# Kernel optimization log

Measured on AMD Instinct MI355X. Metric: run time of the kernel, lower is better.

Reference implementation:

```python
import jax, jax.numpy as jnp
import numpy as np

TAU = 0.05


def _normalize(x):
    return x / jnp.linalg.norm(x, axis=-1, keepdims=True)


def setup_inputs() -> dict:
    key = jax.random.key(0)
    ks = jax.random.split(key, 7)
    D, S, Q, N, P = 256, 64, 4096, 16384, 1024
    return {
        "article_emb": jax.random.normal(ks[0], (D,), dtype=jnp.float32),
        "section_embs": jax.random.normal(ks[1], (S, D), dtype=jnp.float32),
        "question_embs": jax.random.normal(ks[2], (Q, D), dtype=jnp.float32),
        "sentence_embs": jax.random.normal(ks[3], (N, D), dtype=jnp.float32),
        "paragraph_idx_for_question": jax.random.randint(ks[4], (Q,), 0, P, dtype=jnp.int32),
        "section_idx_for_question": jax.random.randint(ks[5], (Q,), 0, S, dtype=jnp.int32),
        "sent_paragraph_idx": jax.random.randint(ks[6], (N,), 0, P, dtype=jnp.int32),
        "num_paragraphs": P,
    }


def reference(article_emb, section_embs, question_embs, sentence_embs,
              paragraph_idx_for_question, section_idx_for_question,
              sent_paragraph_idx, num_paragraphs):
    tau = TAU
    dt = question_embs.dtype
    # normalize (article is normalized in the original but unused in the loss; AT_loss == 0)
    _ = _normalize(article_emb)
    sec = _normalize(section_embs)   # [S, D]
    que = _normalize(question_embs)  # [Q, D]
    sen = _normalize(sentence_embs)  # [N, D]
    Q, N = que.shape[0], sen.shape[0]
    S = sec.shape[0]

    # ---------- QS debiased InfoNCE ----------
    sim_qs = jnp.matmul(que, sen.T) / tau              # [Q, N]
    exp_qs = jnp.exp(sim_qs)                           # [Q, N]
    pos = paragraph_idx_for_question[:, None] == sent_paragraph_idx[None, :]  # [Q, N]
    M = pos.sum(axis=1)                                # positives per question
    Nn = N - M                                         # negatives per question
    sum_pos = jnp.where(pos, exp_qs, 0.0).sum(axis=1)
    sum_neg = exp_qs.sum(axis=1) - sum_pos
    eta_plus = 1.0 / max(int(num_paragraphs), 1)
    eta_minus = 1.0 - eta_plus
    min_val = jnp.exp(jnp.asarray(-1.0 / tau, dtype=dt))
    M_f = jnp.maximum(M, 1).astype(dt)
    Nn_f = jnp.maximum(Nn, 1).astype(dt)
    g = jnp.maximum((sum_neg / Nn_f - eta_plus * sum_pos / M_f) / eta_minus, min_val)  # [Q]
    valid = (M > 0) & (Nn > 0)                         # [Q]
    # -log(numer / (numer + N_neg * g)) = -(sim - log(denom))
    denom_qs = exp_qs + (Nn.astype(dt) * g)[:, None]
    log_ratio_qs = sim_qs - jnp.log(denom_qs)
    mask_qs = pos & valid[:, None]
    total_qs = jnp.where(valid, M, 0).sum()
    qs_loss = -jnp.where(mask_qs, log_ratio_qs, 0.0).sum()
    qs_loss = jnp.where(total_qs > 0, qs_loss / total_qs.astype(dt), jnp.asarray(0.0, dt))

    # ---------- SQ InfoNCE ----------
    sim_sq = jnp.matmul(sec, que.T) / tau              # [S, Q]
    exp_sq = jnp.exp(sim_sq)
    posq = section_idx_for_question[None, :] == jnp.arange(S)[:, None]  # [S, Q]
    Mq = posq.sum(axis=1)
    Nnq = Q - Mq
    sum_neg_q = exp_sq.sum(axis=1) - jnp.where(posq, exp_sq, 0.0).sum(axis=1)  # [S]
    log_ratio_sq = sim_sq - jnp.log(exp_sq + sum_neg_q[:, None])
    validq = (Mq > 0) & (Nnq > 0)
    mask_sq = posq & validq[:, None]
    total_sq = jnp.where(validq, Mq, 0).sum()
    sq_loss = -jnp.where(mask_sq, log_ratio_sq, 0.0).sum()
    sq_loss = jnp.where(total_sq > 0, sq_loss / total_sq.astype(dt), jnp.asarray(0.0, dt))

    return qs_loss + sq_loss
```

## Files before the change

kernel.cpp:

```cpp
#include <hip/hip_runtime.h>
#include <hip/hip_bf16.h>
#include <math.h>

#define D 256
#define INV_TAU 20.0f
#define CAP 64
#define PBUF 128

typedef __attribute__((ext_vector_type(4))) float f32x4;
typedef __attribute__((ext_vector_type(8))) short bf16x8_t;

#define GLOAD16(gp, lp) \
    __builtin_amdgcn_global_load_lds((const __attribute__((address_space(1))) void*)(gp), \
                                     (__attribute__((address_space(3))) void*)(lp), 16, 0, 0)

__device__ __forceinline__ unsigned short f2bf(float f) {
    union { float f; unsigned u; } v; v.f = f;
    unsigned r = v.u + 0x7FFFu + ((v.u >> 16) & 1u);
    return (unsigned short)(r >> 16);
}

__global__ void norm_all(const float* __restrict__ que, const float* __restrict__ sen,
                         const float* __restrict__ sec,
                         unsigned short* __restrict__ queb, unsigned short* __restrict__ senb,
                         unsigned short* __restrict__ secb, int Q, int N, int S) {
    int r = blockIdx.x * 4 + (threadIdx.x >> 6);
    int lane = threadIdx.x & 63;
    if (r >= Q + N + S) return;
    const float* src; unsigned short* dst; int row;
    if (r < Q) { src = que; dst = queb; row = r; }
    else if (r < Q + N) { src = sen; dst = senb; row = r - Q; }
    else { src = sec; dst = secb; row = r - Q - N; }
    const float4* p = (const float4*)(src + (size_t)row * D);
    float4 v = p[lane];
    float ss = v.x * v.x + v.y * v.y + v.z * v.z + v.w * v.w;
    #pragma unroll
    for (int m = 1; m < 64; m <<= 1) ss += __shfl_xor(ss, m);
    float rn = rsqrtf(ss);
    ushort4 o;
    o.x = f2bf(v.x * rn); o.y = f2bf(v.y * rn); o.z = f2bf(v.z * rn); o.w = f2bf(v.w * rn);
    *(ushort4*)(dst + (size_t)row * D + lane * 4) = o;
}

__global__ __launch_bounds__(256, 4)
void qs_sq(const unsigned short* __restrict__ queb, const unsigned short* __restrict__ senb,
           const unsigned short* __restrict__ secb,
           const int* __restrict__ pidq, const int* __restrict__ pidn,
           const int* __restrict__ sidx, int Q,
           float* __restrict__ partial, int* __restrict__ cnt, float* __restrict__ pos_s,
           float* __restrict__ sq_all, float* __restrict__ sq_pos, int* __restrict__ sq_m,
           float* __restrict__ simq) {
    __shared__ unsigned short As[2][128 * 32];
    __shared__ unsigned short Bs[2][128 * 32];
    __shared__ int pqs[128];
    __shared__ int pns[128];
    __shared__ float sums[2][128];
    __shared__ int lcnt;
    __shared__ int lq[PBUF];
    __shared__ float lsv[PBUF];

    const int tid = threadIdx.x;
    const int lane = tid & 63;
    const int cl = lane & 15;
    const int g = lane >> 4;
    const int wid = tid >> 6;
    const int bid = blockIdx.x;
    const int nsq = Q >> 7;

    if (bid < nsq) {
        const int q0 = bid * 128;
        const int qw = q0 + wid * 32;
        f32x4 acc[4][2];
        #pragma unroll
        for (int si = 0; si < 4; ++si)
            #pragma unroll
            for (int qi = 0; qi < 2; ++qi)
                acc[si][qi] = (f32x4){0.f, 0.f, 0.f, 0.f};
        const unsigned short* abase = secb + (size_t)cl * D + g * 8;
        const unsigned short* bbase = queb + (size_t)(qw + cl) * D + g * 8;
        #pragma unroll
        for (int kk = 0; kk < 8; ++kk) {
            const int k0 = kk * 32;
            bf16x8_t af[4], bq[2];
            #pragma unroll
            for (int si = 0; si < 4; ++si)
                af[si] = *(const bf16x8_t*)(abase + si * 16 * D + k0);
            #pragma unroll
            for (int qi = 0; qi < 2; ++qi)
                bq[qi] = *(const bf16x8_t*)(bbase + qi * 16 * D + k0);
            #pragma unroll
            for (int si = 0; si < 4; ++si)
                #pragma unroll
                for (int qi = 0; qi < 2; ++qi)
                    acc[si][qi] = __builtin_amdgcn_mfma_f32_16x16x32_bf16(af[si], bq[qi], acc[si][qi], 0, 0, 0);
        }
        int sidxv[2];
        sidxv[0] = sidx[qw + cl];
        sidxv[1] = sidx[qw + 16 + cl];
        #pragma unroll
        for (int si = 0; si < 4; ++si) {
            float pa[4] = {0.f, 0.f, 0.f, 0.f};
            #pragma unroll
            for (int qi = 0; qi < 2; ++qi) {
                #pragma unroll
                for (int j = 0; j < 4; ++j) {
                    int srow = si * 16 + g * 4 + j;
                    float sv = acc[si][qi][j] * INV_TAU;
                    float e = __expf(sv);
                    pa[j] += e;
                    if (sidxv[qi] == srow) {
                        int q = qw + qi * 16 + cl;
                        simq[q] = sv;
                        atomicAdd(&sq_pos[srow], e);
                        atomicAdd(&sq_m[srow], 1);
                    }
                }
            }
            #pragma unroll
            for (int j = 0; j < 4; ++j) {
                float a = pa[j];
                #pragma unroll
                for (int msk = 1; msk < 16; msk <<= 1) a += __shfl_xor(a, msk);
                if (cl == 0) atomicAdd(&sq_all[si * 16 + g * 4 + j], a);
            }
        }
        return;
    }

    const int qbid = bid - nsq;
    const int xcd = qbid & 7;
    const int loc = qbid >> 3;
    const int qt = loc & 31;
    const int nt = xcd * 16 + (loc >> 5);
    const int wr = wid >> 1, wc = wid & 1;
    const int n0 = nt * 128;
    const int q0 = qt * 128;

    if (tid < 128) pqs[tid] = pidq[q0 + tid];
    else           pns[tid - 128] = pidn[n0 + tid - 128];
    if (tid == 0) lcnt = 0;
    __syncthreads();

    int cid0 = (2 * wid) * 64 + lane;
    int cid1 = (2 * wid + 1) * 64 + lane;
    int r0 = cid0 >> 2, c0 = cid0 & 3;
    int r1 = cid1 >> 2, c1 = cid1 & 3;
    const unsigned short* qa0 = queb + (size_t)(q0 + r0) * D + ((c0 ^ ((r0 >> 1) & 3)) << 3);
    const unsigned short* qa1 = queb + (size_t)(q0 + r1) * D + ((c1 ^ ((r1 >> 1) & 3)) << 3);
    const unsigned short* sb0 = senb + (size_t)(n0 + r0) * D + ((c0 ^ ((r0 >> 1) & 3)) << 3);
    const unsigned short* sb1 = senb + (size_t)(n0 + r1) * D + ((c1 ^ ((r1 >> 1) & 3)) << 3);
    const int ld0 = (2 * wid) * 512;
    const int ld1 = (2 * wid + 1) * 512;

#define STAGE(buf, k0) do { \
    GLOAD16(qa0 + (k0), &As[buf][ld0]); \
    GLOAD16(qa1 + (k0), &As[buf][ld1]); \
    GLOAD16(sb0 + (k0), &Bs[buf][ld0]); \
    GLOAD16(sb1 + (k0), &Bs[buf][ld1]); \
} while (0)

    f32x4 acc[4][4];
    #pragma unroll
    for (int m = 0; m < 4; ++m)
        #pragma unroll
        for (int n = 0; n < 4; ++n)
            acc[m][n] = (f32x4){0.f, 0.f, 0.f, 0.f};

    int offA[4], offB[4];
    #pragma unroll
    for (int m = 0; m < 4; ++m) {
        int r = wr * 64 + m * 16 + cl;
        offA[m] = r * 32 + ((g ^ ((r >> 1) & 3)) << 3);
    }
    #pragma unroll
    for (int n = 0; n < 4; ++n) {
        int r = wc * 64 + n * 16 + cl;
        offB[n] = r * 32 + ((g ^ ((r >> 1) & 3)) << 3);
    }

    STAGE(0, 0);
    #pragma unroll
    for (int ks = 0; ks < 8; ++ks) {
        const int cur = ks & 1;
        if (ks < 7) {
            STAGE(cur ^ 1, (ks + 1) * 32);
            asm volatile("s_waitcnt vmcnt(4)" ::: "memory");
        } else {
            asm volatile("s_waitcnt vmcnt(0)" ::: "memory");
        }
        __builtin_amdgcn_s_barrier();
        bf16x8_t af[4], bg[4];
        #pragma unroll
        for (int m = 0; m < 4; ++m) af[m] = *(const bf16x8_t*)&As[cur][offA[m]];
        #pragma unroll
        for (int n = 0; n < 4; ++n) bg[n] = *(const bf16x8_t*)&Bs[cur][offB[n]];
        #pragma unroll
        for (int m = 0; m < 4; ++m)
            #pragma unroll
            for (int n = 0; n < 4; ++n)
                acc[m][n] = __builtin_amdgcn_mfma_f32_16x16x32_bf16(af[m], bg[n], acc[m][n], 0, 0, 0);
        if (ks < 7) __builtin_amdgcn_s_barrier();
    }
#undef STAGE

    #pragma unroll
    for (int m = 0; m < 4; ++m) {
        float se[4] = {0.f, 0.f, 0.f, 0.f};
        int pqr[4];
        #pragma unroll
        for (int j = 0; j < 4; ++j) pqr[j] = pqs[wr * 64 + m * 16 + g * 4 + j];
        #pragma unroll
        for (int n = 0; n < 4; ++n) {
            const int pcol = pns[wc * 64 + n * 16 + cl];
            #pragma unroll
            for (int j = 0; j < 4; ++j) {
                float s = acc[m][n][j] * INV_TAU;
                float e = __expf(s);
                se[j] += e;
                if (pqr[j] == pcol) {
                    int li = atomicAdd(&lcnt, 1);
                    if (li < PBUF) { lq[li] = q0 + wr * 64 + m * 16 + g * 4 + j; lsv[li] = s; }
                }
            }
        }
        #pragma unroll
        for (int j = 0; j < 4; ++j) {
            float a = se[j];
            #pragma unroll
            for (int msk = 1; msk < 16; msk <<= 1) a += __shfl_xor(a, msk);
            if (cl == 0) sums[wc][wr * 64 + m * 16 + g * 4 + j] = a;
        }
    }
    __syncthreads();
    if (tid < 128)
        partial[(size_t)nt * Q + q0 + tid] = sums[0][tid] + sums[1][tid];
    int nc = lcnt < PBUF ? lcnt : PBUF;
    for (int i = tid; i < nc; i += 256) {
        int q = lq[i];
        int idx = atomicAdd(&cnt[q], 1);
        if (idx < CAP) pos_s[(size_t)q * CAP + idx] = lsv[i];
    }
}

__global__ __launch_bounds__(256)
void finish(const float* __restrict__ partial, int NB,
            const int* __restrict__ cnt, const float* __restrict__ pos_s,
            const int* __restrict__ sidx, const float* __restrict__ simq,
            const float* __restrict__ sq_all, const float* __restrict__ sq_pos,
            const int* __restrict__ sq_m,
            const int* __restrict__ npp, int Qn, int Ntot,
            float* __restrict__ bpart) {
    __shared__ float fred[4][4];
    const int tid = threadIdx.x, lane = tid & 63, wid = tid >> 6;
    const int q = blockIdx.x * 4 + wid;

    float Sa = 0.f;
    for (int nb = lane; nb < NB; nb += 64) Sa += partial[(size_t)nb * Qn + q];
    #pragma unroll
    for (int m = 1; m < 64; m <<= 1) Sa += __shfl_xor(Sa, m);

    int M = cnt[q];
    int mc = M < CAP ? M : CAP;
    float s = 0.f, e = 0.f;
    if (lane < mc) { s = pos_s[(size_t)q * CAP + lane]; e = __expf(s); }
    float Sp = e;
    #pragma unroll
    for (int m = 1; m < 64; m <<= 1) Sp += __shfl_xor(Sp, m);

    int Nn = Ntot - M;
    int P = npp[0];
    float eta_p = 1.0f / (float)(P > 1 ? P : 1);
    float eta_m = 1.0f - eta_p;
    float Mf = (float)(M > 1 ? M : 1);
    float Nnf = (float)(Nn > 1 ? Nn : 1);
    float gg = fmaxf(((Sa - Sp) / Nnf - eta_p * Sp / Mf) / eta_m, __expf(-INV_TAU));
    float c = (float)Nn * gg;

    float contrib = (lane < mc) ? (s - __logf(e + c)) : 0.f;
    #pragma unroll
    for (int m = 1; m < 64; m <<= 1) contrib += __shfl_xor(contrib, m);

    if (lane == 0) {
        float qs_num = 0.f, qs_cnt = 0.f, sq_num = 0.f, sq_cnt = 0.f;
        if (M > 0 && Nn > 0) { qs_num = contrib; qs_cnt = (float)M; }
        int sct = sidx[q];
        int Mq = sq_m[sct];
        if (Mq > 0 && (Qn - Mq) > 0) {
            float sv = simq[q];
            float sumneg = sq_all[sct] - sq_pos[sct];
            sq_num = sv - __logf(__expf(sv) + sumneg);
            sq_cnt = 1.f;
        }
        fred[wid][0] = qs_num; fred[wid][1] = qs_cnt;
        fred[wid][2] = sq_num; fred[wid][3] = sq_cnt;
    }
    __syncthreads();
    if (tid < 4) {
        float v = fred[0][tid] + fred[1][tid] + fred[2][tid] + fred[3][tid];
        bpart[(size_t)blockIdx.x * 4 + tid] = v;
    }
}

__global__ void combine2(const float* __restrict__ bpart, int nblk, float* __restrict__ out) {
    __shared__ float r2[4][4];
    const int tid = threadIdx.x, lane = tid & 63, wid = tid >> 6;
    float v[4] = {0.f, 0.f, 0.f, 0.f};
    for (int i = tid; i < nblk; i += 256) {
        #pragma unroll
        for (int c2 = 0; c2 < 4; ++c2) v[c2] += bpart[(size_t)i * 4 + c2];
    }
    #pragma unroll
    for (int m = 1; m < 64; m <<= 1)
        #pragma unroll
        for (int c2 = 0; c2 < 4; ++c2) v[c2] += __shfl_xor(v[c2], m);
    if (lane == 0) {
        #pragma unroll
        for (int c2 = 0; c2 < 4; ++c2) r2[wid][c2] = v[c2];
    }
    __syncthreads();
    if (tid == 0) {
        float qs_num = r2[0][0] + r2[1][0] + r2[2][0] + r2[3][0];
        float qs_cnt = r2[0][1] + r2[1][1] + r2[2][1] + r2[3][1];
        float sq_num = r2[0][2] + r2[1][2] + r2[2][2] + r2[3][2];
        float sq_cnt = r2[0][3] + r2[1][3] + r2[2][3] + r2[3][3];
        float qs = qs_cnt > 0.f ? -qs_num / qs_cnt : 0.f;
        float sq = sq_cnt > 0.f ? -sq_num / sq_cnt : 0.f;
        out[0] = qs + sq;
    }
}

extern "C" void kernel_launch(void* const* d_in, const int* in_sizes, int n_in,
                              void* d_out, int out_size, void* d_ws, size_t ws_size,
                              hipStream_t stream) {
    const float* sec = (const float*)d_in[1];
    const float* que = (const float*)d_in[2];
    const float* sen = (const float*)d_in[3];
    const int* pidq = (const int*)d_in[4];
    const int* sidx = (const int*)d_in[5];
    const int* pidn = (const int*)d_in[6];
    const int* npp = (const int*)d_in[7];
    const int S = in_sizes[1] / D;
    const int Q = in_sizes[2] / D;
    const int N = in_sizes[3] / D;
    const int NB = N / 128;
    const int FBLK = Q / 4;

    char* p = (char*)d_ws;
    unsigned short* queb = (unsigned short*)p; p += (size_t)Q * D * 2;
    unsigned short* senb = (unsigned short*)p; p += (size_t)N * D * 2;
    unsigned short* secb = (unsigned short*)p; p += (size_t)S * D * 2;
    float* simq = (float*)p; p += (size_t)Q * 4;
    float* pos_s = (float*)p; p += (size_t)Q * CAP * 4;
    float* partial = (float*)p; p += (size_t)NB * Q * 4;
    float* bpart = (float*)p; p += (size_t)FBLK * 4 * 4;
    char* z0 = p;
    int* cnt = (int*)p; p += (size_t)Q * 4;
    float* sq_all = (float*)p; p += (size_t)S * 4;
    float* sq_pos = (float*)p; p += (size_t)S * 4;
    int* sq_m = (int*)p; p += (size_t)S * 4;
    size_t zbytes = (size_t)(p - z0);

    hipMemsetAsync(z0, 0, zbytes, stream);
    norm_all<<<(Q + N + S + 3) / 4, 256, 0, stream>>>(que, sen, sec, queb, senb, secb, Q, N, S);
    qs_sq<<<Q / 128 + (Q / 128) * NB, 256, 0, stream>>>(queb, senb, secb, pidq, pidn, sidx, Q,
                                                        partial, cnt, pos_s,
                                                        sq_all, sq_pos, sq_m, simq);
    finish<<<FBLK, 256, 0, stream>>>(partial, NB, cnt, pos_s, sidx, simq,
                                     sq_all, sq_pos, sq_m, npp, Q, N, bpart);
    combine2<<<1, 256, 0, stream>>>(bpart, FBLK, (float*)d_out);
}
```

Measured before the change: 96.02 us.

## Process two sentence tiles per block with triple-buffered LDS pipeline

Each QS block now covers 128 questions against 256 sentences (two N tiles), which halves the grid size and reuses the question-row staging across both tiles. The K loop becomes a 16-step pipeline with three LDS buffers and a single barrier per step in place of two. Per-wave partial sums go straight to global memory, which removes the shared-memory reduction but doubles the number of partial slices that finish must read. Occupancy drops from 4 to 3 blocks per SIMD because of the larger LDS footprint. The question tile is still re-fetched from global memory for the second sentence tile.

Result: slower. 113.0 us (+17.7%).

```diff
diff --git a/kernel.cpp b/kernel.cpp
--- a/kernel.cpp
+++ b/kernel.cpp
@@ -5,7 +5,7 @@
 #define D 256
 #define INV_TAU 20.0f
 #define CAP 64
-#define PBUF 128
+#define PBUF 192
 
 typedef __attribute__((ext_vector_type(4))) float f32x4;
 typedef __attribute__((ext_vector_type(8))) short bf16x8_t;
@@ -42,7 +42,7 @@
     *(ushort4*)(dst + (size_t)row * D + lane * 4) = o;
 }
 
-__global__ __launch_bounds__(256, 4)
+__global__ __launch_bounds__(256, 3)
 void qs_sq(const unsigned short* __restrict__ queb, const unsigned short* __restrict__ senb,
            const unsigned short* __restrict__ secb,
            const int* __restrict__ pidq, const int* __restrict__ pidn,
@@ -50,11 +50,10 @@
            float* __restrict__ partial, int* __restrict__ cnt, float* __restrict__ pos_s,
            float* __restrict__ sq_all, float* __restrict__ sq_pos, int* __restrict__ sq_m,
            float* __restrict__ simq) {
-    __shared__ unsigned short As[2][128 * 32];
-    __shared__ unsigned short Bs[2][128 * 32];
+    __shared__ unsigned short As[3][128 * 32];
+    __shared__ unsigned short Bs[3][128 * 32];
     __shared__ int pqs[128];
-    __shared__ int pns[128];
-    __shared__ float sums[2][128];
+    __shared__ int pns[256];
     __shared__ int lcnt;
     __shared__ int lq[PBUF];
     __shared__ float lsv[PBUF];
@@ -131,13 +130,13 @@
     const int xcd = qbid & 7;
     const int loc = qbid >> 3;
     const int qt = loc & 31;
-    const int nt = xcd * 16 + (loc >> 5);
+    const int npair = xcd * 8 + (loc >> 5);
     const int wr = wid >> 1, wc = wid & 1;
-    const int n0 = nt * 128;
+    const int n0 = npair * 256;
     const int q0 = qt * 128;
 
     if (tid < 128) pqs[tid] = pidq[q0 + tid];
-    else           pns[tid - 128] = pidn[n0 + tid - 128];
+    pns[tid] = pidn[n0 + tid];
     if (tid == 0) lcnt = 0;
     __syncthreads();
 
@@ -152,11 +151,13 @@
     const int ld0 = (2 * wid) * 512;
     const int ld1 = (2 * wid + 1) * 512;
 
-#define STAGE(buf, k0) do { \
-    GLOAD16(qa0 + (k0), &As[buf][ld0]); \
-    GLOAD16(qa1 + (k0), &As[buf][ld1]); \
-    GLOAD16(sb0 + (k0), &Bs[buf][ld0]); \
-    GLOAD16(sb1 + (k0), &Bs[buf][ld1]); \
+#define STAGE(buf, sp) do { \
+    const int ka_ = ((sp) & 7) * 32; \
+    const int kb_ = ((sp) >> 3) * 128 * D + ka_; \
+    GLOAD16(qa0 + ka_, &As[buf][ld0]); \
+    GLOAD16(qa1 + ka_, &As[buf][ld1]); \
+    GLOAD16(sb0 + kb_, &Bs[buf][ld0]); \
+    GLOAD16(sb1 + kb_, &Bs[buf][ld1]); \
 } while (0)
 
     f32x4 acc[4][4];
@@ -165,8 +166,11 @@
         #pragma unroll
         for (int n = 0; n < 4; ++n)
             acc[m][n] = (f32x4){0.f, 0.f, 0.f, 0.f};
-
-    int offA[4], offB[4];
+    float se[16];
+    #pragma unroll
+    for (int i = 0; i < 16; ++i) se[i] = 0.f;
+
+    int offA[4], offB[4], pqr[16];
     #pragma unroll
     for (int m = 0; m < 4; ++m) {
         int r = wr * 64 + m * 16 + cl;
@@ -177,18 +181,19 @@
         int r = wc * 64 + n * 16 + cl;
         offB[n] = r * 32 + ((g ^ ((r >> 1) & 3)) << 3);
     }
+    #pragma unroll
+    for (int i = 0; i < 16; ++i)
+        pqr[i] = pqs[wr * 64 + (i >> 2) * 16 + g * 4 + (i & 3)];
 
     STAGE(0, 0);
-    #pragma unroll
-    for (int ks = 0; ks < 8; ++ks) {
-        const int cur = ks & 1;
-        if (ks < 7) {
-            STAGE(cur ^ 1, (ks + 1) * 32);
-            asm volatile("s_waitcnt vmcnt(4)" ::: "memory");
-        } else {
-            asm volatile("s_waitcnt vmcnt(0)" ::: "memory");
-        }
+    STAGE(1, 1);
+    #pragma unroll
+    for (int ks = 0; ks < 16; ++ks) {
+        if (ks == 15) asm volatile("s_waitcnt vmcnt(0)" ::: "memory");
+        else          asm volatile("s_waitcnt vmcnt(4)" ::: "memory");
         __builtin_amdgcn_s_barrier();
+        if (ks <= 13) STAGE((ks + 2) % 3, ks + 2);
+        const int cur = ks % 3;
         bf16x8_t af[4], bg[4];
         #pragma unroll
         for (int m = 0; m < 4; ++m) af[m] = *(const bf16x8_t*)&As[cur][offA[m]];
@@ -199,41 +204,50 @@
             #pragma unroll
             for (int n = 0; n < 4; ++n)
                 acc[m][n] = __builtin_amdgcn_mfma_f32_16x16x32_bf16(af[m], bg[n], acc[m][n], 0, 0, 0);
-        if (ks < 7) __builtin_amdgcn_s_barrier();
-    }
-#undef STAGE
-
-    #pragma unroll
-    for (int m = 0; m < 4; ++m) {
-        float se[4] = {0.f, 0.f, 0.f, 0.f};
-        int pqr[4];
-        #pragma unroll
-        for (int j = 0; j < 4; ++j) pqr[j] = pqs[wr * 64 + m * 16 + g * 4 + j];
-        #pragma unroll
-        for (int n = 0; n < 4; ++n) {
-            const int pcol = pns[wc * 64 + n * 16 + cl];
-            #pragma unroll
-            for (int j = 0; j < 4; ++j) {
-                float s = acc[m][n][j] * INV_TAU;
-                float e = __expf(s);
-                se[j] += e;
-                if (pqr[j] == pcol) {
-                    int li = atomicAdd(&lcnt, 1);
-                    if (li < PBUF) { lq[li] = q0 + wr * 64 + m * 16 + g * 4 + j; lsv[li] = s; }
+
+        if (ks == 7 || ks == 15) {
+            const int tile = ks >> 3;
+            #pragma unroll
+            for (int m = 0; m < 4; ++m) {
+                #pragma unroll
+                for (int n = 0; n < 4; ++n) {
+                    const int pcol = pns[tile * 128 + wc * 64 + n * 16 + cl];
+                    #pragma unroll
+                    for (int j = 0; j < 4; ++j) {
+                        float s = acc[m][n][j] * INV_TAU;
+                        float e = __expf(s);
+                        se[m * 4 + j] += e;
+                        if (pqr[m * 4 + j] == pcol) {
+                            int li = atomicAdd(&lcnt, 1);
+                            if (li < PBUF) {
+                                lq[li] = q0 + wr * 64 + m * 16 + g * 4 + j;
+                                lsv[li] = s;
+                            }
+                        }
+                    }
                 }
             }
+            const int slice = (npair * 2 + tile) * 2 + wc;
+            #pragma unroll
+            for (int i = 0; i < 16; ++i) {
+                float a = se[i];
+                #pragma unroll
+                for (int msk = 1; msk < 16; msk <<= 1) a += __shfl_xor(a, msk);
+                if (cl == 0)
+                    partial[(size_t)slice * Q + q0 + wr * 64 + (i >> 2) * 16 + g * 4 + (i & 3)] = a;
+            }
+            #pragma unroll
+            for (int m = 0; m < 4; ++m)
+                #pragma unroll
+                for (int n = 0; n < 4; ++n)
+                    acc[m][n] = (f32x4){0.f, 0.f, 0.f, 0.f};
+            #pragma unroll
+            for (int i = 0; i < 16; ++i) se[i] = 0.f;
         }
-        #pragma unroll
-        for (int j = 0; j < 4; ++j) {
-            float a = se[j];
-            #pragma unroll
-            for (int msk = 1; msk < 16; msk <<= 1) a += __shfl_xor(a, msk);
-            if (cl == 0) sums[wc][wr * 64 + m * 16 + g * 4 + j] = a;
-        }
-    }
+    }
+#undef STAGE
+
     __syncthreads();
-    if (tid < 128)
-        partial[(size_t)nt * Q + q0 + tid] = sums[0][tid] + sums[1][tid];
     int nc = lcnt < PBUF ? lcnt : PBUF;
     for (int i = tid; i < nc; i += 256) {
         int q = lq[i];
@@ -243,7 +257,7 @@
 }
 
 __global__ __launch_bounds__(256)
-void finish(const float* __restrict__ partial, int NB,
+void finish(const float* __restrict__ partial, int NSLICE,
             const int* __restrict__ cnt, const float* __restrict__ pos_s,
             const int* __restrict__ sidx, const float* __restrict__ simq,
             const float* __restrict__ sq_all, const float* __restrict__ sq_pos,
@@ -255,7 +269,7 @@
     const int q = blockIdx.x * 4 + wid;
 
     float Sa = 0.f;
-    for (int nb = lane; nb < NB; nb += 64) Sa += partial[(size_t)nb * Qn + q];
+    for (int nb = lane; nb < NSLICE; nb += 64) Sa += partial[(size_t)nb * Qn + q];
     #pragma unroll
     for (int m = 1; m < 64; m <<= 1) Sa += __shfl_xor(Sa, m);
 
@@ -342,7 +356,7 @@
     const int S = in_sizes[1] / D;
     const int Q = in_sizes[2] / D;
     const int N = in_sizes[3] / D;
-    const int NB = N / 128;
+    const int NSLICE = (N / 128) * 2;
     const int FBLK = Q / 4;
 
     char* p = (char*)d_ws;
@@ -351,7 +365,7 @@
     unsigned short* secb = (unsigned short*)p; p += (size_t)S * D * 2;
     float* simq = (float*)p; p += (size_t)Q * 4;
     float* pos_s = (float*)p; p += (size_t)Q * CAP * 4;
-    float* partial = (float*)p; p += (size_t)NB * Q * 4;
+    float* partial = (float*)p; p += (size_t)NSLICE * Q * 4;
     float* bpart = (float*)p; p += (size_t)FBLK * 4 * 4;
     char* z0 = p;
     int* cnt = (int*)p; p += (size_t)Q * 4;
@@ -362,10 +376,10 @@
 
     hipMemsetAsync(z0, 0, zbytes, stream);
     norm_all<<<(Q + N + S + 3) / 4, 256, 0, stream>>>(que, sen, sec, queb, senb, secb, Q, N, S);
-    qs_sq<<<Q / 128 + (Q / 128) * NB, 256, 0, stream>>>(queb, senb, secb, pidq, pidn, sidx, Q,
-                                                        partial, cnt, pos_s,
-                                                        sq_all, sq_pos, sq_m, simq);
-    finish<<<FBLK, 256, 0, stream>>>(partial, NB, cnt, pos_s, sidx, simq,
+    qs_sq<<<Q / 128 + (Q / 128) * (N / 256), 256, 0, stream>>>(queb, senb, secb, pidq, pidn,
+                                                               sidx, Q, partial, cnt, pos_s,
+                                                               sq_all, sq_pos, sq_m, simq);
+    finish<<<FBLK, 256, 0, stream>>>(partial, NSLICE, cnt, pos_s, sidx, simq,
                                      sq_all, sq_pos, sq_m, npp, Q, N, bpart);
     combine2<<<1, 256, 0, stream>>>(bpart, FBLK, (float*)d_out);
 }
```

## Replace double-buffered K32 staging with single-buffer K64 tiles and exp2 epilogue

Applied to the files above, without the earlier changes.

The QS GEMM loop now stages 64-wide K slices into a single LDS buffer with a new XOR swizzle, replacing the 32-wide double-buffered pipeline. This halves the number of barrier rounds and issues larger loads per stage, but loads no longer overlap with MFMA work. The XCD-aware block remapping is dropped in favour of a plain linear mapping. The epilogue computes exp via a hardware exp2 intrinsic with a prescaled constant instead of a multiply followed by __expf.

After: 103.7 us. 8.0% more time.

```diff
diff --git a/kernel.cpp b/kernel.cpp
--- a/kernel.cpp
+++ b/kernel.cpp
@@ -6,6 +6,7 @@
 #define INV_TAU 20.0f
 #define CAP 64
 #define PBUF 128
+#define K2 (20.0f * 1.442695040888963f)
 
 typedef __attribute__((ext_vector_type(4))) float f32x4;
 typedef __attribute__((ext_vector_type(8))) short bf16x8_t;
@@ -50,8 +51,8 @@
            float* __restrict__ partial, int* __restrict__ cnt, float* __restrict__ pos_s,
            float* __restrict__ sq_all, float* __restrict__ sq_pos, int* __restrict__ sq_m,
            float* __restrict__ simq) {
-    __shared__ unsigned short As[2][128 * 32];
-    __shared__ unsigned short Bs[2][128 * 32];
+    __shared__ unsigned short As[128 * 64];
+    __shared__ unsigned short Bs[128 * 64];
     __shared__ int pqs[128];
     __shared__ int pns[128];
     __shared__ float sums[2][128];
@@ -128,36 +129,27 @@
     }
 
     const int qbid = bid - nsq;
-    const int xcd = qbid & 7;
-    const int loc = qbid >> 3;
-    const int qt = loc & 31;
-    const int nt = xcd * 16 + (loc >> 5);
+    const int qt = qbid & 31;
+    const int nt = qbid >> 5;
     const int wr = wid >> 1, wc = wid & 1;
+    const int q0 = qt * 128;
     const int n0 = nt * 128;
-    const int q0 = qt * 128;
 
     if (tid < 128) pqs[tid] = pidq[q0 + tid];
     else           pns[tid - 128] = pidn[n0 + tid - 128];
     if (tid == 0) lcnt = 0;
-    __syncthreads();
-
-    int cid0 = (2 * wid) * 64 + lane;
-    int cid1 = (2 * wid + 1) * 64 + lane;
-    int r0 = cid0 >> 2, c0 = cid0 & 3;
-    int r1 = cid1 >> 2, c1 = cid1 & 3;
-    const unsigned short* qa0 = queb + (size_t)(q0 + r0) * D + ((c0 ^ ((r0 >> 1) & 3)) << 3);
-    const unsigned short* qa1 = queb + (size_t)(q0 + r1) * D + ((c1 ^ ((r1 >> 1) & 3)) << 3);
-    const unsigned short* sb0 = senb + (size_t)(n0 + r0) * D + ((c0 ^ ((r0 >> 1) & 3)) << 3);
-    const unsigned short* sb1 = senb + (size_t)(n0 + r1) * D + ((c1 ^ ((r1 >> 1) & 3)) << 3);
-    const int ld0 = (2 * wid) * 512;
-    const int ld1 = (2 * wid + 1) * 512;
-
-#define STAGE(buf, k0) do { \
-    GLOAD16(qa0 + (k0), &As[buf][ld0]); \
-    GLOAD16(qa1 + (k0), &As[buf][ld1]); \
-    GLOAD16(sb0 + (k0), &Bs[buf][ld0]); \
-    GLOAD16(sb1 + (k0), &Bs[buf][ld1]); \
-} while (0)
+
+    const int srow = tid >> 3;
+    const int sch = (tid & 7) ^ (srow & 7);
+    const unsigned short* qa = queb + (size_t)(q0 + srow) * D + sch * 8;
+    const unsigned short* sb = senb + (size_t)(n0 + srow) * D + sch * 8;
+
+#define STAGE(k0) do { \
+    _Pragma("unroll") \
+    for (int j_ = 0; j_ < 4; ++j_) { \
+        GLOAD16(qa + (k0) + j_ * 32 * D, &As[j_ * 2048 + wid * 512]); \
+        GLOAD16(sb + (k0) + j_ * 32 * D, &Bs[j_ * 2048 + wid * 512]); \
+    } } while (0)
 
     f32x4 acc[4][4];
     #pragma unroll
@@ -166,40 +158,40 @@
         for (int n = 0; n < 4; ++n)
             acc[m][n] = (f32x4){0.f, 0.f, 0.f, 0.f};
 
-    int offA[4], offB[4];
+    int offA0[4], offB0[4];
     #pragma unroll
     for (int m = 0; m < 4; ++m) {
         int r = wr * 64 + m * 16 + cl;
-        offA[m] = r * 32 + ((g ^ ((r >> 1) & 3)) << 3);
+        offA0[m] = r * 64 + ((g ^ (cl & 7)) << 3);
     }
     #pragma unroll
     for (int n = 0; n < 4; ++n) {
         int r = wc * 64 + n * 16 + cl;
-        offB[n] = r * 32 + ((g ^ ((r >> 1) & 3)) << 3);
-    }
-
-    STAGE(0, 0);
-    #pragma unroll
-    for (int ks = 0; ks < 8; ++ks) {
-        const int cur = ks & 1;
-        if (ks < 7) {
-            STAGE(cur ^ 1, (ks + 1) * 32);
-            asm volatile("s_waitcnt vmcnt(4)" ::: "memory");
-        } else {
-            asm volatile("s_waitcnt vmcnt(0)" ::: "memory");
-        }
-        __builtin_amdgcn_s_barrier();
-        bf16x8_t af[4], bg[4];
-        #pragma unroll
-        for (int m = 0; m < 4; ++m) af[m] = *(const bf16x8_t*)&As[cur][offA[m]];
-        #pragma unroll
-        for (int n = 0; n < 4; ++n) bg[n] = *(const bf16x8_t*)&Bs[cur][offB[n]];
-        #pragma unroll
-        for (int m = 0; m < 4; ++m)
-            #pragma unroll
-            for (int n = 0; n < 4; ++n)
-                acc[m][n] = __builtin_amdgcn_mfma_f32_16x16x32_bf16(af[m], bg[n], acc[m][n], 0, 0, 0);
-        if (ks < 7) __builtin_amdgcn_s_barrier();
+        offB0[n] = r * 64 + ((g ^ (cl & 7)) << 3);
+    }
+
+    STAGE(0);
+    #pragma unroll
+    for (int ks = 0; ks < 4; ++ks) {
+        __syncthreads();
+        #pragma unroll
+        for (int kk = 0; kk < 2; ++kk) {
+            const int kx = kk << 5;
+            bf16x8_t af[4], bg[4];
+            #pragma unroll
+            for (int m = 0; m < 4; ++m) af[m] = *(const bf16x8_t*)&As[offA0[m] ^ kx];
+            #pragma unroll
+            for (int n = 0; n < 4; ++n) bg[n] = *(const bf16x8_t*)&Bs[offB0[n] ^ kx];
+            #pragma unroll
+            for (int m = 0; m < 4; ++m)
+                #pragma unroll
+                for (int n = 0; n < 4; ++n)
+                    acc[m][n] = __builtin_amdgcn_mfma_f32_16x16x32_bf16(af[m], bg[n], acc[m][n], 0, 0, 0);
+        }
+        if (ks < 3) {
+            __syncthreads();
+            STAGE((ks + 1) * 64);
+        }
     }
 #undef STAGE
 
@@ -214,12 +206,14 @@
             const int pcol = pns[wc * 64 + n * 16 + cl];
             #pragma unroll
             for (int j = 0; j < 4; ++j) {
-                float s = acc[m][n][j] * INV_TAU;
-                float e = __expf(s);
+                float e = __builtin_amdgcn_exp2f(acc[m][n][j] * K2);
                 se[j] += e;
                 if (pqr[j] == pcol) {
                     int li = atomicAdd(&lcnt, 1);
-                    if (li < PBUF) { lq[li] = q0 + wr * 64 + m * 16 + g * 4 + j; lsv[li] = s; }
+                    if (li < PBUF) {
+                        lq[li] = q0 + wr * 64 + m * 16 + g * 4 + j;
+                        lsv[li] = acc[m][n][j] * INV_TAU;
+                    }
                 }
             }
         }
@@ -243,7 +237,7 @@
 }
 
 __global__ __launch_bounds__(256)
-void finish(const float* __restrict__ partial, int NB,
+void finish(const float* __restrict__ partial, int NSLICE,
             const int* __restrict__ cnt, const float* __restrict__ pos_s,
             const int* __restrict__ sidx, const float* __restrict__ simq,
             const float* __restrict__ sq_all, const float* __restrict__ sq_pos,
@@ -255,7 +249,7 @@
     const int q = blockIdx.x * 4 + wid;
 
     float Sa = 0.f;
-    for (int nb = lane; nb < NB; nb += 64) Sa += partial[(size_t)nb * Qn + q];
+    for (int nb = lane; nb < NSLICE; nb += 64) Sa += partial[(size_t)nb * Qn + q];
     #pragma unroll
     for (int m = 1; m < 64; m <<= 1) Sa += __shfl_xor(Sa, m);
 
```
